# Performance work log

Measured on AMD Instinct MI355X. Metric: run time of the kernel, lower is better.

The kernel has to match this reference:

```python
import jax, jax.numpy as jnp
import numpy as np

F = 128          # gnn_out_features
D = 2 * F        # GNN_Emb width (mu || logvar)
N_SRC, N_DST = 50000, 10000
N_CATE, P = 18, 8
E = 100000
TAU = 1.0        # decay time constant (get_decay_weight assumed exp(-dt/tau))


def setup_inputs() -> dict:
    key = jax.random.key(0)
    ks = jax.random.split(key, 8)
    return {
        "gnn_emb_src": jax.random.normal(ks[0], (N_SRC, D), dtype=jnp.float32),
        "gnn_emb_dst": jax.random.normal(ks[1], (N_DST, D), dtype=jnp.float32),
        "news_pref": jax.random.normal(ks[2], (N_DST, N_CATE, P, D), dtype=jnp.float32),
        "last_update_time": jax.random.uniform(ks[3], (N_DST, N_CATE, P), dtype=jnp.float32),
        "time": jax.random.uniform(ks[4], (E,), dtype=jnp.float32),
        "cate_id": jax.random.randint(ks[5], (N_SRC,), 0, N_CATE),
        "src_idx": jax.random.randint(ks[6], (E,), 0, N_SRC),
        "dst_idx": jax.random.randint(ks[7], (E,), 0, N_DST),
    }


def reference(gnn_emb_src, gnn_emb_dst, news_pref, last_update_time,
              time, cate_id, src_idx, dst_idx):
    # --- per-edge gathers (DGL edges.src / edges.dst) ---
    src_emb = gnn_emb_src[src_idx, :F]                 # Representation, sample<=0  [E, F]
    cate = cate_id[src_idx]                            # [E]
    lut = last_update_time[dst_idx, cate]              # category-specific       [E, P]
    pref = news_pref[dst_idx, cate]                    # category-specific       [E, P, D]

    # --- decay-weighted fusion ---
    delta_t = time[0] - lut                            # Time[0] - Last_Update_Time [E, P]
    w = jnp.exp(-delta_t / TAU)                        # get_decay_weight         [E, P]
    target = gnn_emb_dst[dst_idx][:, None, :]          # dst GNN_Emb broadcast    [E, 1, D]
    decayed = pref * w[..., None] + target * (1.0 - w[..., None])  # [E, P, D]
    pref_emb = decayed[..., :F]                        # mu half, sample<=0       [E, P, F]

    # --- scaled dot-product attention: query=src_emb over P pref slots ---
    scores = jnp.einsum('ef,epf->ep', src_emb, pref_emb) / jnp.sqrt(jnp.float32(F))
    attn = jax.nn.softmax(scores, axis=-1)             # [E, P]
    dst_pref_emb = jnp.einsum('ep,epf->ef', attn, pref_emb)  # [E, F]

    # --- edge score ---
    return jnp.sum(src_emb * dst_pref_emb, axis=1)     # [E]
```

## Files before the change

### kernel.cpp

```cpp
#include <hip/hip_runtime.h>
#include <math.h>

#define F 128
#define D 256
#define N_CATE 18
#define P 8

__global__ __launch_bounds__(256) void score_predictor_kernel(
    const float* __restrict__ gnn_emb_src,
    const float* __restrict__ gnn_emb_dst,
    const float* __restrict__ news_pref,
    const float* __restrict__ last_update,
    const float* __restrict__ time_arr,
    const int*   __restrict__ cate_id,
    const int*   __restrict__ src_idx,
    const int*   __restrict__ dst_idx,
    float* __restrict__ out,
    int E)
{
    const int wave = (int)((blockIdx.x * blockDim.x + threadIdx.x) >> 6);
    const int lane = (int)(threadIdx.x & 63);
    if (wave >= E) return;
    const int e = wave;
    const int p = lane >> 3;
    const int j = lane & 7;

    const int s = src_idx[e];
    const int d = dst_idx[e];
    const int c = cate_id[s];
    const float t0 = time_arr[0];

    const float* __restrict__ srow = gnn_emb_src + (size_t)s * D;
    const float* __restrict__ drow = gnn_emb_dst + (size_t)d * D;
    const size_t dc = (size_t)d * N_CATE + (size_t)c;
    const float* __restrict__ prow = news_pref + dc * (size_t)(P * D) + (size_t)p * D;

    const float wp = __expf(last_update[dc * P + p] - t0);
    const float omw = 1.0f - wp;

    float qp = 0.0f, tp = 0.0f;
#pragma unroll
    for (int k = 0; k < 4; ++k) {
        const int off = k * 32 + j * 4;
        const float4 sv = *(const float4*)(srow + off);
        const float4 dv = *(const float4*)(drow + off);
        const float4 pv = *(const float4*)(prow + off);
        qp += sv.x * pv.x + sv.y * pv.y + sv.z * pv.z + sv.w * pv.w;
        tp += sv.x * dv.x + sv.y * dv.y + sv.z * dv.z + sv.w * dv.w;
    }

#pragma unroll
    for (int m = 1; m <= 4; m <<= 1) {
        qp += __shfl_xor(qp, m, 64);
        tp += __shfl_xor(tp, m, 64);
    }

    const float inv_sqrtF = 0.088388347648318447f;
    const float sp = (wp * qp + omw * tp) * inv_sqrtF;

    float mx = sp;
#pragma unroll
    for (int m = 8; m <= 32; m <<= 1) {
        mx = fmaxf(mx, __shfl_xor(mx, m, 64));
    }

    const float ep = __expf(sp - mx);
    float num = ep * sp;
    float den = ep;
#pragma unroll
    for (int m = 8; m <= 32; m <<= 1) {
        num += __shfl_xor(num, m, 64);
        den += __shfl_xor(den, m, 64);
    }

    if (lane == 0) {
        out[e] = (num / den) * 11.313708498984761f;
    }
}

extern "C" void kernel_launch(void* const* d_in, const int* in_sizes, int n_in,
                              void* d_out, int out_size, void* d_ws, size_t ws_size,
                              hipStream_t stream) {
    const float* gnn_emb_src = (const float*)d_in[0];
    const float* gnn_emb_dst = (const float*)d_in[1];
    const float* news_pref   = (const float*)d_in[2];
    const float* last_update = (const float*)d_in[3];
    const float* time_arr    = (const float*)d_in[4];
    const int*   cate_id     = (const int*)d_in[5];
    const int*   src_idx     = (const int*)d_in[6];
    const int*   dst_idx     = (const int*)d_in[7];
    float* out = (float*)d_out;

    const int E = in_sizes[6];
    const int waves_per_block = 256 / 64;
    const int grid = (E + waves_per_block - 1) / waves_per_block;

    score_predictor_kernel<<<grid, 256, 0, stream>>>(
        gnn_emb_src, gnn_emb_dst, news_pref, last_update, time_arr,
        cate_id, src_idx, dst_idx, out, E);
}
```

Measured before the change: 79.70 us.

## Sort edges by (dst,cate) key and remap blocks to XCD-contiguous ranges

Adds a counting sort pipeline (zero, histogram, three-pass scan, scatter) that orders edges by their dst*N_CATE+cate key, and the main kernel processes edges in that order. It also remaps block IDs so that each XCD handles a contiguous range of sorted edges. Edges sharing a news_pref row (8 KB) then run on the same XCD and can hit in its L2 instead of refetching from HBM. The cost is six extra kernel launches and atomics over 100K edges and 180K keys, plus scattered output writes and an indirect load through the order array.

```diff
diff --git a/kernel.cpp b/kernel.cpp
--- a/kernel.cpp
+++ b/kernel.cpp
@@ -5,6 +5,86 @@
 #define D 256
 #define N_CATE 18
 #define P 8
+
+
+__global__ void zero_kernel(int* __restrict__ p, int n) {
+    int i = blockIdx.x * blockDim.x + threadIdx.x;
+    if (i < n) p[i] = 0;
+}
+
+__global__ void hist_kernel(const int* __restrict__ src_idx,
+                            const int* __restrict__ dst_idx,
+                            const int* __restrict__ cate_id,
+                            int* __restrict__ keys, int* __restrict__ cnt, int E) {
+    int e = blockIdx.x * blockDim.x + threadIdx.x;
+    if (e >= E) return;
+    int s = src_idx[e];
+    int k = dst_idx[e] * N_CATE + cate_id[s];
+    keys[e] = k;
+    atomicAdd(&cnt[k], 1);
+}
+
+__global__ __launch_bounds__(256) void scan_block_totals(const int* __restrict__ cnt,
+                                                         int* __restrict__ blk, int nkey) {
+    int b = blockIdx.x, t = threadIdx.x;
+    int lane = t & 63, wid = t >> 6;
+    int base = b * 1024 + t * 4;
+    int s = 0;
+#pragma unroll
+    for (int i = 0; i < 4; ++i) { int idx = base + i; if (idx < nkey) s += cnt[idx]; }
+#pragma unroll
+    for (int m = 1; m < 64; m <<= 1) s += __shfl_xor(s, m, 64);
+    __shared__ int lds[4];
+    if (lane == 0) lds[wid] = s;
+    __syncthreads();
+    if (t == 0) blk[b] = lds[0] + lds[1] + lds[2] + lds[3];
+}
+
+__global__ __launch_bounds__(256) void scan_totals(int* __restrict__ blk, int nblk) {
+    int t = threadIdx.x, lane = t & 63, wid = t >> 6;
+    int v = (t < nblk) ? blk[t] : 0;
+    int x = v;
+#pragma unroll
+    for (int m = 1; m < 64; m <<= 1) { int y = __shfl_up(x, m, 64); if (lane >= m) x += y; }
+    __shared__ int lds[4];
+    if (lane == 63) lds[wid] = x;
+    __syncthreads();
+    int off = 0;
+    for (int w = 0; w < wid; ++w) off += lds[w];
+    if (t < nblk) blk[t] = x - v + off;
+}
+
+__global__ __launch_bounds__(256) void scan_apply(int* __restrict__ cnt,
+                                                  const int* __restrict__ blk, int nkey) {
+    int b = blockIdx.x, t = threadIdx.x;
+    int lane = t & 63, wid = t >> 6;
+    int base = b * 1024 + t * 4;
+    int c[4]; int ts = 0;
+#pragma unroll
+    for (int i = 0; i < 4; ++i) { int idx = base + i; c[i] = (idx < nkey) ? cnt[idx] : 0; ts += c[i]; }
+    int x = ts;
+#pragma unroll
+    for (int m = 1; m < 64; m <<= 1) { int y = __shfl_up(x, m, 64); if (lane >= m) x += y; }
+    __shared__ int lds[4];
+    if (lane == 63) lds[wid] = x;
+    __syncthreads();
+    int off = blk[b];
+    for (int w = 0; w < wid; ++w) off += lds[w];
+    int excl = off + x - ts;
+#pragma unroll
+    for (int i = 0; i < 4; ++i) {
+        int idx = base + i;
+        if (idx < nkey) { cnt[idx] = excl; excl += c[i]; }
+    }
+}
+
+__global__ void scatter_kernel(const int* __restrict__ keys, int* __restrict__ cnt,
+                               int* __restrict__ order, int E) {
+    int e = blockIdx.x * blockDim.x + threadIdx.x;
+    if (e >= E) return;
+    int pos = atomicAdd(&cnt[keys[e]], 1);
+    order[pos] = e;
+}
 
 __global__ __launch_bounds__(256) void score_predictor_kernel(
     const float* __restrict__ gnn_emb_src,
@@ -15,13 +95,21 @@
     const int*   __restrict__ cate_id,
     const int*   __restrict__ src_idx,
     const int*   __restrict__ dst_idx,
+    const int*   __restrict__ order,
     float* __restrict__ out,
     int E)
 {
-    const int wave = (int)((blockIdx.x * blockDim.x + threadIdx.x) >> 6);
+    const int B = (int)gridDim.x;
+    const int bid = (int)blockIdx.x;
+    const int q = B >> 3, r = B & 7;
+    const int xcd = bid & 7, pos = bid >> 3;
+    const int nb = (xcd < r) ? (xcd * (q + 1)) : (r * (q + 1) + (xcd - r) * q);
+    const int sb = nb + pos;
+
+    const int w = sb * 4 + (int)(threadIdx.x >> 6);
     const int lane = (int)(threadIdx.x & 63);
-    if (wave >= E) return;
-    const int e = wave;
+    if (w >= E) return;
+    const int e = order ? order[w] : w;
     const int p = lane >> 3;
     const int j = lane & 7;
 
@@ -92,10 +180,31 @@
     float* out = (float*)d_out;
 
     const int E = in_sizes[6];
+    const int N_DST = in_sizes[1] / D;
+    const int nkey = N_DST * N_CATE;
+    const int nblk = (nkey + 1023) / 1024;
+
+    const size_t need = ((size_t)nkey + 256 + 2 * (size_t)E) * sizeof(int);
+    int* order = nullptr;
+
+    if (ws_size >= need && nblk <= 256) {
+        int* cnt  = (int*)d_ws;
+        int* blk  = cnt + nkey;
+        int* keys = blk + 256;
+        order     = keys + E;
+
+        zero_kernel<<<(nkey + 255) / 256, 256, 0, stream>>>(cnt, nkey);
+        hist_kernel<<<(E + 255) / 256, 256, 0, stream>>>(src_idx, dst_idx, cate_id, keys, cnt, E);
+        scan_block_totals<<<nblk, 256, 0, stream>>>(cnt, blk, nkey);
+        scan_totals<<<1, 256, 0, stream>>>(blk, nblk);
+        scan_apply<<<nblk, 256, 0, stream>>>(cnt, blk, nkey);
+        scatter_kernel<<<(E + 255) / 256, 256, 0, stream>>>(keys, cnt, order, E);
+    }
+
     const int waves_per_block = 256 / 64;
     const int grid = (E + waves_per_block - 1) / waves_per_block;
 
     score_predictor_kernel<<<grid, 256, 0, stream>>>(
         gnn_emb_src, gnn_emb_dst, news_pref, last_update, time_arr,
-        cate_id, src_idx, dst_idx, out, E);
-}
+        cate_id, src_idx, dst_idx, order, out, E);
+}
```

Result: slower. 106.5 us (+33.6%).

## Counting-sort edges by destination and remap blocks per XCD for cache locality

Applied to the files above, without the earlier changes.

Adds a histogram, single-block scan and atomic scatter pass that groups edges by destination node, storing the source, packed dst/category key and original edge id. The main kernel then walks edges in sorted order and remaps block ids so that contiguous ranges of sorted edges land on the same XCD. The aim is to reuse gnn_emb_dst rows and news_pref slices in each XCD's L2. The cost is three extra kernel launches plus a memset, atomic contention in the scatter, and a serial single-block scan.

```diff
diff --git a/kernel.cpp b/kernel.cpp
--- a/kernel.cpp
+++ b/kernel.cpp
@@ -5,6 +5,63 @@
 #define D 256
 #define N_CATE 18
 #define P 8
+
+
+__global__ void hist_kernel(const int* __restrict__ dst_idx,
+                            int* __restrict__ cnt, int E) {
+    int e = blockIdx.x * blockDim.x + threadIdx.x;
+    if (e < E) atomicAdd(&cnt[dst_idx[e]], 1);
+}
+
+__global__ __launch_bounds__(1024) void scan_kernel(int* __restrict__ cnt, int nkey) {
+    const int t = threadIdx.x;
+    const int per = (nkey + 1023) >> 10;
+    const int base = t * per;
+    int ts = 0;
+    for (int i = 0; i < per; ++i) {
+        int idx = base + i;
+        if (idx < nkey) ts += cnt[idx];
+    }
+    int x = ts;
+    const int lane = t & 63;
+#pragma unroll
+    for (int m = 1; m < 64; m <<= 1) {
+        int y = __shfl_up(x, m, 64);
+        if (lane >= m) x += y;
+    }
+    __shared__ int wsum[16];
+    if (lane == 63) wsum[t >> 6] = x;
+    __syncthreads();
+    int off = 0;
+    for (int w0 = 0; w0 < (t >> 6); ++w0) off += wsum[w0];
+    int excl = off + x - ts;
+    for (int i = 0; i < per; ++i) {
+        int idx = base + i;
+        if (idx < nkey) {
+            int v = cnt[idx];
+            cnt[idx] = excl;
+            excl += v;
+        }
+    }
+}
+
+__global__ void scatter_kernel(const int* __restrict__ src_idx,
+                               const int* __restrict__ dst_idx,
+                               const int* __restrict__ cate_id,
+                               int* __restrict__ cnt,
+                               int* __restrict__ s_sorted,
+                               int* __restrict__ k_sorted,
+                               int* __restrict__ e_sorted, int E) {
+    int e = blockIdx.x * blockDim.x + threadIdx.x;
+    if (e >= E) return;
+    int d = dst_idx[e];
+    int s = src_idx[e];
+    int c = cate_id[s];
+    int pos = atomicAdd(&cnt[d], 1);
+    s_sorted[pos] = s;
+    k_sorted[pos] = (d << 5) | c;
+    e_sorted[pos] = e;
+}
 
 __global__ __launch_bounds__(256) void score_predictor_kernel(
     const float* __restrict__ gnn_emb_src,
@@ -15,19 +72,39 @@
     const int*   __restrict__ cate_id,
     const int*   __restrict__ src_idx,
     const int*   __restrict__ dst_idx,
+    const int*   __restrict__ s_sorted,
+    const int*   __restrict__ k_sorted,
+    const int*   __restrict__ e_sorted,
     float* __restrict__ out,
     int E)
 {
-    const int wave = (int)((blockIdx.x * blockDim.x + threadIdx.x) >> 6);
+    const int B = (int)gridDim.x;
+    const int bid = (int)blockIdx.x;
+    const int q = B >> 3, r = B & 7;
+    const int xcd = bid & 7, pos = bid >> 3;
+    const int nb = (xcd < r) ? (xcd * (q + 1)) : (r * (q + 1) + (xcd - r) * q);
+    const int sb = nb + pos;
+
+    const int w = sb * 4 + (int)(threadIdx.x >> 6);
     const int lane = (int)(threadIdx.x & 63);
-    if (wave >= E) return;
-    const int e = wave;
+    if (w >= E) return;
+
+    int s, d, c, e;
+    if (s_sorted) {
+        s = s_sorted[w];
+        const int k = k_sorted[w];
+        e = e_sorted[w];
+        d = k >> 5;
+        c = k & 31;
+    } else {
+        e = w;
+        s = src_idx[e];
+        d = dst_idx[e];
+        c = cate_id[s];
+    }
+
     const int p = lane >> 3;
     const int j = lane & 7;
-
-    const int s = src_idx[e];
-    const int d = dst_idx[e];
-    const int c = cate_id[s];
     const float t0 = time_arr[0];
 
     const float* __restrict__ srow = gnn_emb_src + (size_t)s * D;
@@ -92,10 +169,28 @@
     float* out = (float*)d_out;
 
     const int E = in_sizes[6];
+    const int N_DST = in_sizes[1] / D;
+
+    const size_t need = ((size_t)N_DST + 3 * (size_t)E) * sizeof(int);
+
+    int *s_sorted = nullptr, *k_sorted = nullptr, *e_sorted = nullptr;
+    if (ws_size >= need && N_DST <= 16384 && N_DST < (1 << 14) + 1) {
+        int* cnt = (int*)d_ws;
+        s_sorted = cnt + N_DST;
+        k_sorted = s_sorted + E;
+        e_sorted = k_sorted + E;
+
+        hipMemsetAsync(cnt, 0, (size_t)N_DST * sizeof(int), stream);
+        hist_kernel<<<(E + 255) / 256, 256, 0, stream>>>(dst_idx, cnt, E);
+        scan_kernel<<<1, 1024, 0, stream>>>(cnt, N_DST);
+        scatter_kernel<<<(E + 255) / 256, 256, 0, stream>>>(
+            src_idx, dst_idx, cate_id, cnt, s_sorted, k_sorted, e_sorted, E);
+    }
+
     const int waves_per_block = 256 / 64;
     const int grid = (E + waves_per_block - 1) / waves_per_block;
 
     score_predictor_kernel<<<grid, 256, 0, stream>>>(
         gnn_emb_src, gnn_emb_dst, news_pref, last_update, time_arr,
-        cate_id, src_idx, dst_idx, out, E);
+        cate_id, src_idx, dst_idx, s_sorted, k_sorted, e_sorted, out, E);
 }
```

Result: slower. 110.2 us (+38.3%).
